# Kernel optimization log

Hardware: AMD Instinct MI355X
Metric: run time of the kernel (lower is better)

## Reference

```python
import jax, jax.numpy as jnp
import numpy as np
from jax import lax

DIM = 128
HEADS = 8
HEAD_DIM = DIM // HEADS
SR = 2
B, H, W = 2, 80, 80
SCALE = HEAD_DIM ** (-0.5)
BN_EPS = 1e-5


def _conv1x1(x, w, b):
    # x: (B,C,H,W), w: (O,C), b: (O,)
    return jnp.einsum('bchw,oc->bohw', x, w) + b[None, :, None, None]


def setup_inputs() -> dict:
    key = jax.random.key(0)
    ks = jax.random.split(key, 12)
    s = DIM ** -0.5
    x = jax.random.normal(ks[0], (B, DIM, H, W), dtype=jnp.float32)
    q_w = jax.random.normal(ks[1], (DIM, DIM), dtype=jnp.float32) * s
    q_b = jnp.zeros((DIM,), jnp.float32)
    k_w = jax.random.normal(ks[2], (DIM, DIM), dtype=jnp.float32) * s
    k_b = jnp.zeros((DIM,), jnp.float32)
    v_w = jax.random.normal(ks[3], (DIM, DIM), dtype=jnp.float32) * s
    v_b = jnp.zeros((DIM,), jnp.float32)
    sr_w = jax.random.normal(ks[4], (DIM, DIM, SR, SR), dtype=jnp.float32) * (s / SR)
    sr_b = jnp.zeros((DIM,), jnp.float32)
    bn_gamma = jnp.ones((DIM,), jnp.float32)
    bn_beta = jnp.zeros((DIM,), jnp.float32)
    bn_mean = jnp.zeros((DIM,), jnp.float32)
    bn_var = jnp.ones((DIM,), jnp.float32)
    proj_w = jax.random.normal(ks[5], (DIM, DIM), dtype=jnp.float32) * s
    proj_b = jnp.zeros((DIM,), jnp.float32)
    return dict(x=x, q_w=q_w, q_b=q_b, k_w=k_w, k_b=k_b, v_w=v_w, v_b=v_b,
                sr_w=sr_w, sr_b=sr_b, bn_gamma=bn_gamma, bn_beta=bn_beta,
                bn_mean=bn_mean, bn_var=bn_var, proj_w=proj_w, proj_b=proj_b)


def reference(x, q_w, q_b, k_w, k_b, v_w, v_b, sr_w, sr_b,
              bn_gamma, bn_beta, bn_mean, bn_var, proj_w, proj_b):
    b, c, h, w = x.shape
    n = h * w
    # q: (B,h,N,d)
    q = _conv1x1(x, q_w, q_b).reshape(b, HEADS, HEAD_DIM, n).transpose(0, 1, 3, 2)
    # spatial reduction: Conv2d(k=SR, s=SR) + BN(eval) + ReLU
    x_kv = lax.conv_general_dilated(x, sr_w, window_strides=(SR, SR),
                                    padding='VALID',
                                    dimension_numbers=('NCHW', 'OIHW', 'NCHW'))
    x_kv = x_kv + sr_b[None, :, None, None]
    inv = bn_gamma / jnp.sqrt(bn_var + BN_EPS)
    x_kv = x_kv * inv[None, :, None, None] + (bn_beta - bn_mean * inv)[None, :, None, None]
    x_kv = jax.nn.relu(x_kv)
    n_kv = x_kv.shape[2] * x_kv.shape[3]
    k = _conv1x1(x_kv, k_w, k_b).reshape(b, HEADS, HEAD_DIM, n_kv).transpose(0, 1, 3, 2)
    v = _conv1x1(x_kv, v_w, v_b).reshape(b, HEADS, HEAD_DIM, n_kv).transpose(0, 1, 3, 2)
    # explicit attention: (B,h,N,N_kv)
    attn = jnp.einsum('bhnd,bhmd->bhnm', q, k) * SCALE
    attn = jax.nn.softmax(attn, axis=-1)
    out = jnp.einsum('bhnm,bhmd->bhnd', attn, v)  # (B,h,N,d)
    # faithful to source layout: transpose(1,2) then reshape to (B,C,H,W)
    out = out.transpose(0, 2, 1, 3).reshape(b, c, h, w)
    out = _conv1x1(out, proj_w, proj_b)
    return out
```

## Files before the change

### kernel.cpp

```cpp
#include <hip/hip_runtime.h>
#include <hip/hip_bf16.h>
#include <cmath>

#define DIM 128
#define HEADS 8
#define NBATCH 2
#define NQ 6400
#define NKV 1600
#define NC 50
#define BN_EPS 1e-5f
#define LOG2E 1.4426950408889634f

typedef __bf16 bf16_t;
typedef __attribute__((ext_vector_type(8))) __bf16 bf16x8;
typedef __attribute__((ext_vector_type(16))) float f32x16;

union BF8U { bf16x8 v; unsigned u[4]; };

__device__ inline unsigned packbf2(float a, float b) {
  union { __hip_bfloat162 v; unsigned u; } r;
  r.v = __float22bfloat162_rn(make_float2(a, b));
  return r.u;
}

__device__ inline unsigned short f2bf(float v) {
  unsigned u = __float_as_uint(v);
  return (unsigned short)((u + 0x7FFFu + ((u >> 16) & 1u)) >> 16);
}

__global__ __launch_bounds__(256) void prep_all(
    const float* __restrict__ x,
    const float* __restrict__ qw, const float* __restrict__ kw,
    const float* __restrict__ vw, const float* __restrict__ pw,
    const float* __restrict__ srw,
    unsigned short* __restrict__ Xb,
    unsigned short* __restrict__ Wb,
    unsigned short* __restrict__ X4b,
    unsigned short* __restrict__ Vp)
{
  int t = threadIdx.x;
  int bx = blockIdx.x;
  if (bx < 1600) {
    __shared__ float tile[32][33];
    int tx = t & 31, ty = t >> 5;
    int b = bx / 800;
    int rem = bx % 800;
    int c0 = (rem / 200) * 32, s0 = (rem % 200) * 32;
#pragma unroll
    for (int r = 0; r < 32; r += 8)
      tile[ty + r][tx] = x[((size_t)b * DIM + c0 + ty + r) * NQ + s0 + tx];
    __syncthreads();
#pragma unroll
    for (int r = 0; r < 32; r += 8)
      Xb[((size_t)b * NQ + s0 + ty + r) * DIM + c0 + tx] = f2bf(tile[tx][ty + r]);
    return;
  }
  if (bx < 2240) {
    __shared__ float itile[16][164];
    int idx0 = bx - 1600;
    int b  = idx0 / 320;
    int rem = idx0 % 320;
    int i  = rem / 8;
    int c0 = (rem % 8) * 16;
    const float* xb = x + ((size_t)b * DIM + c0) * NQ + (size_t)i * 160;
#pragma unroll
    for (int k = 0; k < 10; ++k) {
      int idx = t + k * 256;
      int r = idx / 160, col = idx % 160;
      itile[r][col] = xb[(size_t)r * NQ + col];
    }
    __syncthreads();
    unsigned short* ob = X4b + ((size_t)b * NKV + (size_t)i * 40) * 512 + c0 * 4;
#pragma unroll
    for (int k = 0; k < 10; ++k) {
      int idx = t + k * 256;
      int j = idx >> 6, cc = idx & 63;
      int cr = cc >> 2, ky = (cc >> 1) & 1, kx = cc & 1;
      ob[(size_t)j * 512 + cc] = f2bf(itile[cr][ky * 80 + 2 * j + kx]);
    }
    return;
  }
  int e = (bx - 2240) * 256 + t;
  if (e < 131072) {
    const float* src; int idx;
    if (e < 16384)      { src = qw;  idx = e; }
    else if (e < 32768) { src = kw;  idx = e - 16384; }
    else if (e < 49152) { src = vw;  idx = e - 32768; }
    else if (e < 65536) { src = pw;  idx = e - 49152; }
    else                { src = srw; idx = e - 65536; }
    Wb[e] = f2bf(src[idx]);
  }
  if (e < NBATCH * HEADS * NC * 32) {
    int cid = e >> 5;
    int pos = e & 31;
    size_t addr = (size_t)cid * 1024 + 256 + ((pos & 16) ? 512 : 0) + (pos & 15);
    Vp[addr] = 0x3F80;
  }
}

__global__ __launch_bounds__(256) void mgemm_qsrkv(
    const bf16_t* __restrict__ Xb, const bf16_t* __restrict__ X4b,
    const bf16_t* __restrict__ Wb,
    const float* __restrict__ q_b, const float* __restrict__ sr_b,
    const float* __restrict__ k_b, const float* __restrict__ v_b,
    const float* __restrict__ bng, const float* __restrict__ bnb,
    const float* __restrict__ bnm, const float* __restrict__ bnv,
    unsigned short* __restrict__ Qb,
    unsigned short* __restrict__ Kp, unsigned short* __restrict__ Vp,
    float sl)
{
  __shared__ __align__(16) unsigned short xs[32][136];
  int t = threadIdx.x;
  int ln = t & 31, hf = (t >> 5) & 1, wid = t >> 6;
  int b = blockIdx.y;
  int o = wid * 32 + ln;

  if (blockIdx.x < 50) {
    int s0 = blockIdx.x * 32;
    const bf16_t* arow = &X4b[((size_t)b * NKV + s0 + ln) * 512 + hf * 8];
    const bf16_t* brow = &Wb[65536 + (size_t)o * 512 + hf * 8];
    f32x16 acc = {};
#pragma unroll 8
    for (int c0 = 0; c0 < 512; c0 += 16) {
      bf16x8 af = *(const bf16x8*)&arow[c0];
      bf16x8 bf = *(const bf16x8*)&brow[c0];
      acc = __builtin_amdgcn_mfma_f32_32x32x16_bf16(af, bf, acc, 0, 0, 0);
    }
    float bv = sr_b[o];
    float inv = bng[o] / sqrtf(bnv[o] + BN_EPS);
    float b2 = bnb[o] - bnm[o] * inv;
#pragma unroll
    for (int g = 0; g < 4; ++g)
#pragma unroll
      for (int j = 0; j < 4; ++j) {
        int s = 8 * g + 4 * hf + j;
        xs[s][o] = f2bf(fmaxf((acc[4 * g + j] + bv) * inv + b2, 0.f));
      }
    __syncthreads();

    const unsigned short* ar2 = &xs[ln][hf * 8];
    const bf16_t* kbrow = &Wb[16384 + (size_t)o * DIM + hf * 8];
    const bf16_t* vbrow = &Wb[32768 + (size_t)o * DIM + hf * 8];
    f32x16 ka = {}, va = {};
#pragma unroll
    for (int c0 = 0; c0 < 128; c0 += 16) {
      bf16x8 af = *(const bf16x8*)&ar2[c0];
      bf16x8 kb = *(const bf16x8*)&kbrow[c0];
      bf16x8 vb = *(const bf16x8*)&vbrow[c0];
      ka = __builtin_amdgcn_mfma_f32_32x32x16_bf16(af, kb, ka, 0, 0, 0);
      va = __builtin_amdgcn_mfma_f32_32x32x16_bf16(af, vb, va, 0, 0, 0);
    }
    int hloc = o >> 4, d = o & 15;
    {
      float kb2 = k_b[o];
      size_t CB = (((size_t)b * HEADS + hloc) * NC + (s0 >> 5)) * 512;
#pragma unroll
      for (int g = 0; g < 4; ++g)
#pragma unroll
        for (int j = 0; j < 4; ++j) {
          int sl2 = 8 * g + 4 * hf + j;
          Kp[CB + sl2 * 16 + d] = f2bf(ka[4 * g + j] + kb2);
        }
    }
    {
      float vb2 = v_b[o];
      size_t CB = (((size_t)b * HEADS + hloc) * NC + (s0 >> 5)) * 1024;
      uint4 w0, w1;
      w0.x = packbf2(va[0] + vb2, va[1] + vb2);
      w0.y = packbf2(va[2] + vb2, va[3] + vb2);
      w0.z = packbf2(va[4] + vb2, va[5] + vb2);
      w0.w = packbf2(va[6] + vb2, va[7] + vb2);
      w1.x = packbf2(va[8] + vb2, va[9] + vb2);
      w1.y = packbf2(va[10] + vb2, va[11] + vb2);
      w1.z = packbf2(va[12] + vb2, va[13] + vb2);
      w1.w = packbf2(va[14] + vb2, va[15] + vb2);
      *(uint4*)&Vp[CB + d * 16 + hf * 8] = w0;
      *(uint4*)&Vp[CB + 512 + d * 16 + hf * 8] = w1;
    }
  } else {
    int s0 = (blockIdx.x - 50) * 32;
    const bf16_t* arow = &Xb[((size_t)b * NQ + s0 + ln) * DIM + hf * 8];
    const bf16_t* brow = &Wb[(size_t)o * DIM + hf * 8];
    f32x16 acc = {};
#pragma unroll
    for (int c0 = 0; c0 < 128; c0 += 16) {
      bf16x8 af = *(const bf16x8*)&arow[c0];
      bf16x8 bf = *(const bf16x8*)&brow[c0];
      acc = __builtin_amdgcn_mfma_f32_32x32x16_bf16(af, bf, acc, 0, 0, 0);
    }
    float bv = q_b[o];
#pragma unroll
    for (int g = 0; g < 4; ++g)
#pragma unroll
      for (int j = 0; j < 4; ++j) {
        int s = s0 + 8 * g + 4 * hf + j;
        Qb[((size_t)b * NQ + s) * DIM + o] = f2bf((acc[4 * g + j] + bv) * sl);
      }
  }
}

__global__ __launch_bounds__(256) void attn_split(
    const bf16_t* __restrict__ Qb, const bf16_t* __restrict__ Kp,
    const bf16_t* __restrict__ Vp, unsigned short* __restrict__ Pb,
    float* __restrict__ Lsum)
{
  const int t = threadIdx.x;
  const int ln = t & 31, hf = (t >> 5) & 1, wid = t >> 6;
  const int h = blockIdx.y;
  const int b = blockIdx.z & 1, half = blockIdx.z >> 1;
  const int q0 = blockIdx.x * 128 + wid * 32;

  bf16x8 qf = *(const bf16x8*)&Qb[((size_t)b * NQ + q0 + ln) * DIM + h * 16 + hf * 8];
  const int bh = b * HEADS + h;
  const bf16_t* kc = &Kp[((size_t)bh * NC + half * 25) * 512 + ln * 16 + hf * 8];
  const bf16_t* vc = &Vp[((size_t)bh * NC + half * 25) * 1024 + ln * 16 + hf * 8];

  f32x16 acc0 = {}, acc1 = {};
  const f32x16 zero = {};

  bf16x8 kf0 = *(const bf16x8*)kc;
  bf16x8 va0 = *(const bf16x8*)vc;
  bf16x8 vb0 = *(const bf16x8*)(vc + 512);
  bf16x8 kf1 = *(const bf16x8*)(kc + 512);
  bf16x8 va1 = *(const bf16x8*)(vc + 1024);
  bf16x8 vb1 = *(const bf16x8*)(vc + 1536);

  f32x16 S0 = __builtin_amdgcn_mfma_f32_32x32x16_bf16(kf0, qf, zero, 0, 0, 0);

  for (int c = 0; c < 25; ++c) {
    int cn = (c + 2 < 25) ? c + 2 : 24;
    bf16x8 kf2 = *(const bf16x8*)(kc + (size_t)cn * 512);
    bf16x8 va2 = *(const bf16x8*)(vc + (size_t)cn * 1024);
    bf16x8 vb2 = *(const bf16x8*)(vc + (size_t)cn * 1024 + 512);

    f32x16 S1 = __builtin_amdgcn_mfma_f32_32x32x16_bf16(kf1, qf, zero, 0, 0, 0);

    BF8U f0, f1;
#pragma unroll
    for (int i = 0; i < 4; ++i) {
      f0.u[i] = packbf2(__builtin_amdgcn_exp2f(S0[2 * i]),
                        __builtin_amdgcn_exp2f(S0[2 * i + 1]));
      f1.u[i] = packbf2(__builtin_amdgcn_exp2f(S0[8 + 2 * i]),
                        __builtin_amdgcn_exp2f(S0[9 + 2 * i]));
    }

    acc0 = __builtin_amdgcn_mfma_f32_32x32x16_bf16(va0, f0.v, acc0, 0, 0, 0);
    acc1 = __builtin_amdgcn_mfma_f32_32x32x16_bf16(vb0, f1.v, acc1, 0, 0, 0);

    S0 = S1;
    kf0 = kf1; va0 = va1; vb0 = vb1;
    kf1 = kf2; va1 = va2; vb1 = vb2;
  }

  f32x16 acc;
#pragma unroll
  for (int i = 0; i < 16; ++i) acc[i] = acc0[i] + acc1[i];

  unsigned short* prow =
      &Pb[(size_t)(half * 2 + b) * (NQ * DIM) + (size_t)(q0 + ln) * DIM + h * 16 + 4 * hf];
  uint2 w0, w1;
  w0.x = packbf2(acc[0], acc[1]); w0.y = packbf2(acc[2], acc[3]);
  w1.x = packbf2(acc[4], acc[5]); w1.y = packbf2(acc[6], acc[7]);
  *(uint2*)&prow[0] = w0;
  *(uint2*)&prow[8] = w1;
  if (!hf)
    Lsum[(size_t)(half * 2 + b) * (HEADS * NQ) + (size_t)h * NQ + q0 + ln] = acc[8];
}

__global__ __launch_bounds__(256) void proj_comb(
    const unsigned short* __restrict__ Pb, const float* __restrict__ Lsum,
    const bf16_t* __restrict__ Wb, const float* __restrict__ p_b,
    float* __restrict__ Out)
{
  __shared__ __align__(16) unsigned short As[32][136];
  int t = threadIdx.x;
  int b = blockIdx.y;
  int s0 = blockIdx.x * 32;

  {
    int tx = t & 31, cg = t >> 5;
#pragma unroll
    for (int it = 0; it < 16; ++it) {
      int c = cg * 16 + it;
      int f = c * NQ + s0 + tx;
      int n = f >> 7, hh = (f >> 4) & 7;
      float p0 = __uint_as_float((unsigned)Pb[(size_t)b * (NQ * DIM) + f] << 16);
      float p1 = __uint_as_float((unsigned)Pb[(size_t)(2 + b) * (NQ * DIM) + f] << 16);
      float L = Lsum[(size_t)b * (HEADS * NQ) + (size_t)hh * NQ + n] +
                Lsum[(size_t)(2 + b) * (HEADS * NQ) + (size_t)hh * NQ + n];
      As[tx][c] = f2bf((p0 + p1) / L);
    }
  }
  __syncthreads();

  int ln = t & 31, hf = (t >> 5) & 1, wid = t >> 6;
  int o = wid * 32 + ln;
  const bf16_t* brow = &Wb[49152 + (size_t)o * DIM + hf * 8];
  const unsigned short* arow = &As[ln][hf * 8];
  f32x16 acc = {};
#pragma unroll
  for (int c0 = 0; c0 < 128; c0 += 16) {
    bf16x8 af = *(const bf16x8*)&arow[c0];
    bf16x8 bf = *(const bf16x8*)&brow[c0];
    acc = __builtin_amdgcn_mfma_f32_32x32x16_bf16(af, bf, acc, 0, 0, 0);
  }
  float bv = p_b[o];
  float* obase = &Out[((size_t)b * DIM + o) * NQ + s0 + 4 * hf];
#pragma unroll
  for (int g = 0; g < 4; ++g) {
    float4 r;
    r.x = acc[4 * g + 0] + bv; r.y = acc[4 * g + 1] + bv;
    r.z = acc[4 * g + 2] + bv; r.w = acc[4 * g + 3] + bv;
    *(float4*)&obase[8 * g] = r;
  }
}

extern "C" void kernel_launch(void* const* d_in, const int* in_sizes, int n_in,
                              void* d_out, int out_size, void* d_ws, size_t ws_size,
                              hipStream_t stream)
{
  const float* x    = (const float*)d_in[0];
  const float* q_w  = (const float*)d_in[1];
  const float* q_b  = (const float*)d_in[2];
  const float* k_w  = (const float*)d_in[3];
  const float* k_b  = (const float*)d_in[4];
  const float* v_w  = (const float*)d_in[5];
  const float* v_b  = (const float*)d_in[6];
  const float* sr_w = (const float*)d_in[7];
  const float* sr_b = (const float*)d_in[8];
  const float* bng  = (const float*)d_in[9];
  const float* bnb  = (const float*)d_in[10];
  const float* bnm  = (const float*)d_in[11];
  const float* bnv  = (const float*)d_in[12];
  const float* p_w  = (const float*)d_in[13];
  const float* p_b  = (const float*)d_in[14];
  float* out = (float*)d_out;

  float* ws = (float*)d_ws;
  bf16_t* Xb   = (bf16_t*)(ws);
  bf16_t* X4b  = (bf16_t*)(ws + 819200);
  bf16_t* Qb   = (bf16_t*)(ws + 1638400);
  bf16_t* Kp   = (bf16_t*)(ws + 2457600);
  bf16_t* Vp   = (bf16_t*)(ws + 2662400);
  float*  Lsum = ws + 3072000;
  bf16_t* Wb   = (bf16_t*)(ws + 3276800);
  bf16_t* Pb   = (bf16_t*)(ws + 3342336);

  const float sl = 0.25f * LOG2E;

  prep_all<<<dim3(2880), dim3(256), 0, stream>>>(
      x, q_w, k_w, v_w, p_w, sr_w,
      (unsigned short*)Xb, (unsigned short*)Wb,
      (unsigned short*)X4b, (unsigned short*)Vp);

  mgemm_qsrkv<<<dim3(250, NBATCH), dim3(256), 0, stream>>>(
      Xb, X4b, Wb, q_b, sr_b, k_b, v_b, bng, bnb, bnm, bnv,
      (unsigned short*)Qb, (unsigned short*)Kp, (unsigned short*)Vp, sl);

  attn_split<<<dim3(NQ / 128, HEADS, 4), dim3(256), 0, stream>>>(
      Qb, Kp, Vp, (unsigned short*)Pb, Lsum);

  proj_comb<<<dim3(200, NBATCH), dim3(256), 0, stream>>>(
      (const unsigned short*)Pb, Lsum, Wb, p_b, out);
}
```

Baseline: 152.0 us.

## Fold fp32-to-bf16 prep kernel into GEMM kernels reading raw inputs

```diff
diff --git a/kernel.cpp b/kernel.cpp
--- a/kernel.cpp
+++ b/kernel.cpp
@@ -28,79 +28,10 @@
   return (unsigned short)((u + 0x7FFFu + ((u >> 16) & 1u)) >> 16);
 }
 
-__global__ __launch_bounds__(256) void prep_all(
+__global__ __launch_bounds__(256) void mgemm_qsrkv(
     const float* __restrict__ x,
     const float* __restrict__ qw, const float* __restrict__ kw,
-    const float* __restrict__ vw, const float* __restrict__ pw,
-    const float* __restrict__ srw,
-    unsigned short* __restrict__ Xb,
-    unsigned short* __restrict__ Wb,
-    unsigned short* __restrict__ X4b,
-    unsigned short* __restrict__ Vp)
-{
-  int t = threadIdx.x;
-  int bx = blockIdx.x;
-  if (bx < 1600) {
-    __shared__ float tile[32][33];
-    int tx = t & 31, ty = t >> 5;
-    int b = bx / 800;
-    int rem = bx % 800;
-    int c0 = (rem / 200) * 32, s0 = (rem % 200) * 32;
-#pragma unroll
-    for (int r = 0; r < 32; r += 8)
-      tile[ty + r][tx] = x[((size_t)b * DIM + c0 + ty + r) * NQ + s0 + tx];
-    __syncthreads();
-#pragma unroll
-    for (int r = 0; r < 32; r += 8)
-      Xb[((size_t)b * NQ + s0 + ty + r) * DIM + c0 + tx] = f2bf(tile[tx][ty + r]);
-    return;
-  }
-  if (bx < 2240) {
-    __shared__ float itile[16][164];
-    int idx0 = bx - 1600;
-    int b  = idx0 / 320;
-    int rem = idx0 % 320;
-    int i  = rem / 8;
-    int c0 = (rem % 8) * 16;
-    const float* xb = x + ((size_t)b * DIM + c0) * NQ + (size_t)i * 160;
-#pragma unroll
-    for (int k = 0; k < 10; ++k) {
-      int idx = t + k * 256;
-      int r = idx / 160, col = idx % 160;
-      itile[r][col] = xb[(size_t)r * NQ + col];
-    }
-    __syncthreads();
-    unsigned short* ob = X4b + ((size_t)b * NKV + (size_t)i * 40) * 512 + c0 * 4;
-#pragma unroll
-    for (int k = 0; k < 10; ++k) {
-      int idx = t + k * 256;
-      int j = idx >> 6, cc = idx & 63;
-      int cr = cc >> 2, ky = (cc >> 1) & 1, kx = cc & 1;
-      ob[(size_t)j * 512 + cc] = f2bf(itile[cr][ky * 80 + 2 * j + kx]);
-    }
-    return;
-  }
-  int e = (bx - 2240) * 256 + t;
-  if (e < 131072) {
-    const float* src; int idx;
-    if (e < 16384)      { src = qw;  idx = e; }
-    else if (e < 32768) { src = kw;  idx = e - 16384; }
-    else if (e < 49152) { src = vw;  idx = e - 32768; }
-    else if (e < 65536) { src = pw;  idx = e - 49152; }
-    else                { src = srw; idx = e - 65536; }
-    Wb[e] = f2bf(src[idx]);
-  }
-  if (e < NBATCH * HEADS * NC * 32) {
-    int cid = e >> 5;
-    int pos = e & 31;
-    size_t addr = (size_t)cid * 1024 + 256 + ((pos & 16) ? 512 : 0) + (pos & 15);
-    Vp[addr] = 0x3F80;
-  }
-}
-
-__global__ __launch_bounds__(256) void mgemm_qsrkv(
-    const bf16_t* __restrict__ Xb, const bf16_t* __restrict__ X4b,
-    const bf16_t* __restrict__ Wb,
+    const float* __restrict__ vw, const float* __restrict__ srw,
     const float* __restrict__ q_b, const float* __restrict__ sr_b,
     const float* __restrict__ k_b, const float* __restrict__ v_b,
     const float* __restrict__ bng, const float* __restrict__ bnb,
@@ -116,15 +47,31 @@
   int o = wid * 32 + ln;
 
   if (blockIdx.x < 50) {
-    int s0 = blockIdx.x * 32;
-    const bf16_t* arow = &X4b[((size_t)b * NKV + s0 + ln) * 512 + hf * 8];
-    const bf16_t* brow = &Wb[65536 + (size_t)o * 512 + hf * 8];
+    int cid = blockIdx.x;
+    int s0 = cid * 32;
+    int s = s0 + ln;
+    int i = s / 40, j = s % 40;
+    const float* xb = x + (size_t)b * DIM * NQ;
+
     f32x16 acc = {};
-#pragma unroll 8
-    for (int c0 = 0; c0 < 512; c0 += 16) {
-      bf16x8 af = *(const bf16x8*)&arow[c0];
-      bf16x8 bf = *(const bf16x8*)&brow[c0];
-      acc = __builtin_amdgcn_mfma_f32_32x32x16_bf16(af, bf, acc, 0, 0, 0);
+#pragma unroll
+    for (int p = 0; p < 4; ++p) {
+      int ky = p >> 1, kx = p & 1;
+      const float* xpos = xb + (2 * i + ky) * 80 + (2 * j + kx);
+      const float* wrow = srw + (size_t)o * 512 + p;
+#pragma unroll
+      for (int c0 = 0; c0 < 128; c0 += 16) {
+        int cb = c0 + hf * 8;
+        BF8U af, bf;
+#pragma unroll
+        for (int m = 0; m < 4; ++m) {
+          af.u[m] = packbf2(xpos[(size_t)(cb + 2 * m) * NQ],
+                            xpos[(size_t)(cb + 2 * m + 1) * NQ]);
+          bf.u[m] = packbf2(wrow[(size_t)(cb + 2 * m) * 4],
+                            wrow[(size_t)(cb + 2 * m + 1) * 4]);
+        }
+        acc = __builtin_amdgcn_mfma_f32_32x32x16_bf16(af.v, bf.v, acc, 0, 0, 0);
+      }
     }
     float bv = sr_b[o];
     float inv = bng[o] / sqrtf(bnv[o] + BN_EPS);
@@ -132,39 +79,47 @@
 #pragma unroll
     for (int g = 0; g < 4; ++g)
 #pragma unroll
-      for (int j = 0; j < 4; ++j) {
-        int s = 8 * g + 4 * hf + j;
-        xs[s][o] = f2bf(fmaxf((acc[4 * g + j] + bv) * inv + b2, 0.f));
+      for (int jj = 0; jj < 4; ++jj) {
+        int sr = 8 * g + 4 * hf + jj;
+        xs[sr][o] = f2bf(fmaxf((acc[4 * g + jj] + bv) * inv + b2, 0.f));
       }
     __syncthreads();
 
     const unsigned short* ar2 = &xs[ln][hf * 8];
-    const bf16_t* kbrow = &Wb[16384 + (size_t)o * DIM + hf * 8];
-    const bf16_t* vbrow = &Wb[32768 + (size_t)o * DIM + hf * 8];
+    const float* kwrow = kw + (size_t)o * DIM;
+    const float* vwrow = vw + (size_t)o * DIM;
     f32x16 ka = {}, va = {};
 #pragma unroll
     for (int c0 = 0; c0 < 128; c0 += 16) {
+      int cb = c0 + hf * 8;
       bf16x8 af = *(const bf16x8*)&ar2[c0];
-      bf16x8 kb = *(const bf16x8*)&kbrow[c0];
-      bf16x8 vb = *(const bf16x8*)&vbrow[c0];
-      ka = __builtin_amdgcn_mfma_f32_32x32x16_bf16(af, kb, ka, 0, 0, 0);
-      va = __builtin_amdgcn_mfma_f32_32x32x16_bf16(af, vb, va, 0, 0, 0);
+      BF8U kb, vb;
+      float4 k0 = *(const float4*)(kwrow + cb);
+      float4 k1 = *(const float4*)(kwrow + cb + 4);
+      float4 v0 = *(const float4*)(vwrow + cb);
+      float4 v1 = *(const float4*)(vwrow + cb + 4);
+      kb.u[0] = packbf2(k0.x, k0.y); kb.u[1] = packbf2(k0.z, k0.w);
+      kb.u[2] = packbf2(k1.x, k1.y); kb.u[3] = packbf2(k1.z, k1.w);
+      vb.u[0] = packbf2(v0.x, v0.y); vb.u[1] = packbf2(v0.z, v0.w);
+      vb.u[2] = packbf2(v1.x, v1.y); vb.u[3] = packbf2(v1.z, v1.w);
+      ka = __builtin_amdgcn_mfma_f32_32x32x16_bf16(af, kb.v, ka, 0, 0, 0);
+      va = __builtin_amdgcn_mfma_f32_32x32x16_bf16(af, vb.v, va, 0, 0, 0);
     }
     int hloc = o >> 4, d = o & 15;
     {
       float kb2 = k_b[o];
-      size_t CB = (((size_t)b * HEADS + hloc) * NC + (s0 >> 5)) * 512;
+      size_t CB = (((size_t)b * HEADS + hloc) * NC + cid) * 512;
 #pragma unroll
       for (int g = 0; g < 4; ++g)
 #pragma unroll
-        for (int j = 0; j < 4; ++j) {
-          int sl2 = 8 * g + 4 * hf + j;
-          Kp[CB + sl2 * 16 + d] = f2bf(ka[4 * g + j] + kb2);
+        for (int jj = 0; jj < 4; ++jj) {
+          int sl2 = 8 * g + 4 * hf + jj;
+          Kp[CB + sl2 * 16 + d] = f2bf(ka[4 * g + jj] + kb2);
         }
     }
     {
       float vb2 = v_b[o];
-      size_t CB = (((size_t)b * HEADS + hloc) * NC + (s0 >> 5)) * 1024;
+      size_t CB = (((size_t)b * HEADS + hloc) * NC + cid) * 1024;
       uint4 w0, w1;
       w0.x = packbf2(va[0] + vb2, va[1] + vb2);
       w0.y = packbf2(va[2] + vb2, va[3] + vb2);
@@ -177,24 +132,39 @@
       *(uint4*)&Vp[CB + d * 16 + hf * 8] = w0;
       *(uint4*)&Vp[CB + 512 + d * 16 + hf * 8] = w1;
     }
+    {
+      int hh = t >> 5, pos = t & 31;
+      size_t addr = (((size_t)b * HEADS + hh) * NC + cid) * 1024 + 256 +
+                    ((pos & 16) ? 512 : 0) + (pos & 15);
+      Vp[addr] = 0x3F80;
+    }
   } else {
     int s0 = (blockIdx.x - 50) * 32;
-    const bf16_t* arow = &Xb[((size_t)b * NQ + s0 + ln) * DIM + hf * 8];
-    const bf16_t* brow = &Wb[(size_t)o * DIM + hf * 8];
+    int s = s0 + ln;
+    const float* xcol = x + (size_t)b * DIM * NQ + s;
+    const float* qwrow = qw + (size_t)o * DIM;
     f32x16 acc = {};
 #pragma unroll
     for (int c0 = 0; c0 < 128; c0 += 16) {
-      bf16x8 af = *(const bf16x8*)&arow[c0];
-      bf16x8 bf = *(const bf16x8*)&brow[c0];
-      acc = __builtin_amdgcn_mfma_f32_32x32x16_bf16(af, bf, acc, 0, 0, 0);
+      int cb = c0 + hf * 8;
+      BF8U af, bf;
+#pragma unroll
+      for (int m = 0; m < 4; ++m)
+        af.u[m] = packbf2(xcol[(size_t)(cb + 2 * m) * NQ],
+                          xcol[(size_t)(cb + 2 * m + 1) * NQ]);
+      float4 b0 = *(const float4*)(qwrow + cb);
+      float4 b1 = *(const float4*)(qwrow + cb + 4);
+      bf.u[0] = packbf2(b0.x, b0.y); bf.u[1] = packbf2(b0.z, b0.w);
+      bf.u[2] = packbf2(b1.x, b1.y); bf.u[3] = packbf2(b1.z, b1.w);
+      acc = __builtin_amdgcn_mfma_f32_32x32x16_bf16(af.v, bf.v, acc, 0, 0, 0);
     }
     float bv = q_b[o];
 #pragma unroll
     for (int g = 0; g < 4; ++g)
 #pragma unroll
-      for (int j = 0; j < 4; ++j) {
-        int s = s0 + 8 * g + 4 * hf + j;
-        Qb[((size_t)b * NQ + s) * DIM + o] = f2bf((acc[4 * g + j] + bv) * sl);
+      for (int jj = 0; jj < 4; ++jj) {
+        int sq = s0 + 8 * g + 4 * hf + jj;
+        Qb[((size_t)b * NQ + sq) * DIM + o] = f2bf((acc[4 * g + jj] + bv) * sl);
       }
   }
 }
@@ -269,7 +239,7 @@
 
 __global__ __launch_bounds__(256) void proj_comb(
     const unsigned short* __restrict__ Pb, const float* __restrict__ Lsum,
-    const bf16_t* __restrict__ Wb, const float* __restrict__ p_b,
+    const float* __restrict__ pw, const float* __restrict__ p_b,
     float* __restrict__ Out)
 {
   __shared__ __align__(16) unsigned short As[32][136];
@@ -295,14 +265,19 @@
 
   int ln = t & 31, hf = (t >> 5) & 1, wid = t >> 6;
   int o = wid * 32 + ln;
-  const bf16_t* brow = &Wb[49152 + (size_t)o * DIM + hf * 8];
+  const float* brow = pw + (size_t)o * DIM;
   const unsigned short* arow = &As[ln][hf * 8];
   f32x16 acc = {};
 #pragma unroll
   for (int c0 = 0; c0 < 128; c0 += 16) {
+    int cb = c0 + hf * 8;
     bf16x8 af = *(const bf16x8*)&arow[c0];
-    bf16x8 bf = *(const bf16x8*)&brow[c0];
-    acc = __builtin_amdgcn_mfma_f32_32x32x16_bf16(af, bf, acc, 0, 0, 0);
+    BF8U bf;
+    float4 b0 = *(const float4*)(brow + cb);
+    float4 b1 = *(const float4*)(brow + cb + 4);
+    bf.u[0] = packbf2(b0.x, b0.y); bf.u[1] = packbf2(b0.z, b0.w);
+    bf.u[2] = packbf2(b1.x, b1.y); bf.u[3] = packbf2(b1.z, b1.w);
+    acc = __builtin_amdgcn_mfma_f32_32x32x16_bf16(af, bf.v, acc, 0, 0, 0);
   }
   float bv = p_b[o];
   float* obase = &Out[((size_t)b * DIM + o) * NQ + s0 + 4 * hf];
@@ -337,29 +312,21 @@
   float* out = (float*)d_out;
 
   float* ws = (float*)d_ws;
-  bf16_t* Xb   = (bf16_t*)(ws);
-  bf16_t* X4b  = (bf16_t*)(ws + 819200);
-  bf16_t* Qb   = (bf16_t*)(ws + 1638400);
-  bf16_t* Kp   = (bf16_t*)(ws + 2457600);
-  bf16_t* Vp   = (bf16_t*)(ws + 2662400);
-  float*  Lsum = ws + 3072000;
-  bf16_t* Wb   = (bf16_t*)(ws + 3276800);
-  bf16_t* Pb   = (bf16_t*)(ws + 3342336);
+  bf16_t* Qb   = (bf16_t*)(ws);
+  bf16_t* Kp   = (bf16_t*)(ws + 819200);
+  bf16_t* Vp   = (bf16_t*)(ws + 1024000);
+  float*  Lsum = ws + 1433600;
+  bf16_t* Pb   = (bf16_t*)(ws + 1638400);
 
   const float sl = 0.25f * LOG2E;
 
-  prep_all<<<dim3(2880), dim3(256), 0, stream>>>(
-      x, q_w, k_w, v_w, p_w, sr_w,
-      (unsigned short*)Xb, (unsigned short*)Wb,
-      (unsigned short*)X4b, (unsigned short*)Vp);
-
   mgemm_qsrkv<<<dim3(250, NBATCH), dim3(256), 0, stream>>>(
-      Xb, X4b, Wb, q_b, sr_b, k_b, v_b, bng, bnb, bnm, bnv,
+      x, q_w, k_w, v_w, sr_w, q_b, sr_b, k_b, v_b, bng, bnb, bnm, bnv,
       (unsigned short*)Qb, (unsigned short*)Kp, (unsigned short*)Vp, sl);
 
   attn_split<<<dim3(NQ / 128, HEADS, 4), dim3(256), 0, stream>>>(
       Qb, Kp, Vp, (unsigned short*)Pb, Lsum);
 
   proj_comb<<<dim3(200, NBATCH), dim3(256), 0, stream>>>(
-      (const unsigned short*)Pb, Lsum, Wb, p_b, out);
-}
+      (const unsigned short*)Pb, Lsum, p_w, p_b, out);
+}
```

New measurement: 158.6 us. +4.3%, slower.
